# Kernel tuning notes

Hardware: AMD Instinct MI355X
Metric: run time of the kernel (lower is better)

The kernel has to match this reference:

```python
import jax, jax.numpy as jnp
import numpy as np

DT = 0.1
EPS = 0.01


def _trans_layer(x, W, b):
    # x: [B, 2U]; W: [U, U]; b: [U]
    U = b.shape[0]
    t = DT / EPS
    u_in, v_in = x[:, :U], x[:, U:]
    act = jnp.tanh(u_in)
    v_star = (v_in + t * act) / (1.0 + t)
    # Block matrix A = [[I, dt*W], [-dt*W^T, I]] -- identical for all samples,
    # so factor/solve ONCE with a multi-RHS solve instead of torch's per-sample batched LU.
    I = jnp.eye(U, dtype=x.dtype)
    A = jnp.block([[I, DT * W], [-DT * W.T, I]])  # [2U, 2U]
    rhs = jnp.concatenate([u_in + DT * b, v_star], axis=1)  # [B, 2U]
    y = jnp.linalg.solve(A, rhs.T).T  # [B, 2U]
    u, v = y[:, :U], y[:, U:]
    u_out = DT * (v @ W.T) - u_in - DT * b
    v_out = -DT * (u @ W) + t * v - v_in - t * act
    return jnp.concatenate([u_out, v_out], axis=1)


def setup_inputs() -> dict:
    key = jax.random.key(0)
    ks = jax.random.split(key, 14)
    B, D_IN, U, D_OUT = 32768, 256, 256, 10

    def lin_w(k, o, i):
        return (jax.random.uniform(k, (o, i), jnp.float32) * 2.0 - 1.0) / np.sqrt(i).astype(np.float32)

    def lin_b(k, o, fan_in):
        return (jax.random.uniform(k, (o,), jnp.float32) * 2.0 - 1.0) / np.sqrt(fan_in).astype(np.float32)

    return {
        'x': jax.random.normal(ks[0], (B, D_IN), jnp.float32),
        'Wi': lin_w(ks[1], U, D_IN), 'bi': lin_b(ks[2], U, D_IN),
        'W1': lin_w(ks[3], U, U), 'b1': lin_b(ks[4], U, U),
        'W2': lin_w(ks[5], U, U), 'b2': lin_b(ks[6], U, U),
        'W3': lin_w(ks[7], U, U), 'b3': lin_b(ks[8], U, U),
        'W4': lin_w(ks[9], U, U), 'b4': lin_b(ks[10], U, U),
        'Wo': lin_w(ks[11], D_OUT, U), 'bo': lin_b(ks[12], D_OUT, U),
    }


def reference(x, Wi, bi, W1, b1, W2, b2, W3, b3, W4, b4, Wo, bo):
    U = W1.shape[0]
    z = x @ Wi.T + bi                       # linearInput
    z = jnp.concatenate([z, jnp.tanh(z)], axis=1)  # [B, 2U]
    for W, b in ((W1, b1), (W2, b2), (W3, b3), (W4, b4)):
        z = _trans_layer(z, W, b)
    z = z[:, :U]
    logits = z @ Wo.T + bo                  # linearOutput
    return jax.nn.softmax(logits, axis=1)
```

## Files before the change

kernel.cpp:

```cpp
#include <hip/hip_runtime.h>
#include <math.h>

#define DTC 0.1f

typedef _Float16 half8 __attribute__((ext_vector_type(8)));
typedef _Float16 half4v __attribute__((ext_vector_type(4)));
typedef float f32x4 __attribute__((ext_vector_type(4)));
typedef float f32x2 __attribute__((ext_vector_type(2)));

__device__ __forceinline__ float fast_tanh(float x) {
  const float e = __expf(2.f * x);
  const float r = __builtin_amdgcn_rcpf(e + 1.f);
  return fmaf(-2.f, r, 1.f);
}


__global__ __launch_bounds__(256) void k_prep(
    const float* __restrict__ W0, const float* __restrict__ W1,
    const float* __restrict__ W2, const float* __restrict__ W3,
    const float* __restrict__ b2, const float* __restrict__ b3,
    const float* __restrict__ b4,
    _Float16* __restrict__ Wh, _Float16* __restrict__ Wt,
    float* __restrict__ crm) {
  const float* Ws[4] = {W0, W1, W2, W3};
  const int bid = blockIdx.x, tid = threadIdx.x;
  if (bid < 128) {
    const int t = bid * 256 + tid;
    const float* W = Ws[(t * 8) >> 16];
    const int off = (t * 8) & 65535;
    const float4 a = *(const float4*)&W[off];
    const float4 b = *(const float4*)&W[off + 4];
    half8 h;
    h[0] = (_Float16)a.x; h[1] = (_Float16)a.y; h[2] = (_Float16)a.z; h[3] = (_Float16)a.w;
    h[4] = (_Float16)b.x; h[5] = (_Float16)b.y; h[6] = (_Float16)b.z; h[7] = (_Float16)b.w;
    *(half8*)&Wh[t * 8] = h;
  } else if (bid < 384) {
    __shared__ float sh[32][33];
    const int b2i = bid - 128;
    const int l = b2i >> 6, t64 = b2i & 63;
    const int r0 = (t64 >> 3) * 32, c0 = (t64 & 7) * 32;
    const float* W = Ws[l];
    const int i = tid >> 5, j = tid & 31;
#pragma unroll
    for (int p = 0; p < 4; ++p)
      sh[p * 8 + i][j] = W[(r0 + p * 8 + i) * 256 + c0 + j];
    __syncthreads();
#pragma unroll
    for (int p = 0; p < 4; ++p)
      Wt[l * 65536 + (c0 + p * 8 + i) * 256 + r0 + j] = (_Float16)sh[j][p * 8 + i];
  } else {
    const int l = bid - 384;
    const float* W = Ws[l];
    const float* b = (l == 0) ? b2 : (l == 1) ? b3 : b4;
    float s = 0.f;
#pragma unroll 8
    for (int k = 0; k < 256; ++k) s = fmaf(b[k], W[k * 256 + tid], s);
    crm[l * 256 + tid] = -0.09f * s;
  }
}

__global__ __launch_bounds__(256) void k_smm3(const _Float16* __restrict__ A,
                                              const _Float16* __restrict__ B,
                                              const _Float16* __restrict__ Eadd,
                                              _Float16* __restrict__ C,
                                              float scale, int addI) {
  const int tid = threadIdx.x, wave = tid >> 6, lane = tid & 63;
  const int quad = lane >> 4, l16 = lane & 15;
  const int l = blockIdx.z;
  const _Float16* Al = A + (size_t)l * 65536;
  const _Float16* Bl = B + (size_t)l * 65536;
  _Float16* Cl = C + (size_t)l * 65536;
  const int m0 = blockIdx.y * 64 + wave * 16, n0 = blockIdx.x * 64;
  f32x4 acc[4] = {};
#pragma unroll
  for (int kt = 0; kt < 8; ++kt) {
    const half8 af = *(const half8*)&Al[(m0 + l16) * 256 + kt * 32 + quad * 8];
#pragma unroll
    for (int ni = 0; ni < 4; ++ni) {
      const half8 bf = *(const half8*)&Bl[(n0 + ni * 16 + l16) * 256 + kt * 32 + quad * 8];
      acc[ni] = __builtin_amdgcn_mfma_f32_16x16x32_f16(af, bf, acc[ni], 0, 0, 0);
    }
  }
#pragma unroll
  for (int ni = 0; ni < 4; ++ni)
#pragma unroll
    for (int r = 0; r < 4; ++r) {
      const int row = m0 + quad * 4 + r, col = n0 + ni * 16 + l16;
      float v = scale * acc[ni][r];
      if (addI) v += (row == col ? 1.f : 0.f) - (float)(Eadd + (size_t)l * 65536)[row * 256 + col];
      Cl[row * 256 + col] = (_Float16)v;
    }
}

__global__ __launch_bounds__(256) void k_pack(
    const _Float16* __restrict__ Ph, const _Float16* __restrict__ Qt,
    const _Float16* __restrict__ Wt, const float* __restrict__ Wi,
    const float* __restrict__ Wo,
    _Float16* __restrict__ PQP, _Float16* __restrict__ RmP,
    _Float16* __restrict__ WiP, _Float16* __restrict__ WoP) {
  const int t = blockIdx.x * 256 + threadIdx.x;
  if (t < 65536) {
    const int l = t >> 14, c = t & 16383;
    const int ntile = c >> 10, kt = (c >> 6) & 15, lb = c & 63;
    const int n = ntile * 16 + (lb & 15);
    const int kq = (lb >> 4) * 8;
    half8 h;
    if (kt < 8) {
      h = *(const half8*)&Ph[(size_t)l * 65536 + n * 256 + kt * 32 + kq];
#pragma unroll
      for (int j = 0; j < 8; ++j) h[j] = -h[j];
    } else {
      h = *(const half8*)&Qt[(size_t)l * 65536 + n * 256 + (kt - 8) * 32 + kq];
    }
    *(half8*)&PQP[(size_t)t * 8] = h;
  } else if (t < 90112) {
    const int tt = t - 65536;
    const int l = tt >> 13, c = tt & 8191;
    const int ntile = c >> 9, kt = (c >> 6) & 7, lb = c & 63;
    const int n = ntile * 16 + (lb & 15);
    const int k0 = kt * 32 + (lb >> 4) * 8;
    half8 h = *(const half8*)&Wt[(size_t)l * 65536 + n * 256 + k0];
#pragma unroll
    for (int j = 0; j < 8; ++j) h[j] = (_Float16)(-0.9f * (float)h[j]);
    *(half8*)&RmP[(size_t)tt * 8] = h;
  } else if (t < 98304) {
    const int c = t - 90112;
    const int ntile = c >> 9, kt = (c >> 6) & 7, lb = c & 63;
    const int n = ntile * 16 + (lb & 15);
    const int k0 = kt * 32 + (lb >> 4) * 8;
    const float4 a = *(const float4*)&Wi[n * 256 + k0];
    const float4 b = *(const float4*)&Wi[n * 256 + k0 + 4];
    half8 h;
    h[0] = (_Float16)a.x; h[1] = (_Float16)a.y; h[2] = (_Float16)a.z; h[3] = (_Float16)a.w;
    h[4] = (_Float16)b.x; h[5] = (_Float16)b.y; h[6] = (_Float16)b.z; h[7] = (_Float16)b.w;
    *(half8*)&WiP[(size_t)c * 8] = h;
  } else {
    const int c = t - 98304;
    const int kt = c >> 6, lb = c & 63;
    const int n = lb & 15;
    const int k0 = kt * 32 + (lb >> 4) * 8;
    half8 h;
#pragma unroll
    for (int j = 0; j < 8; ++j) h[j] = (_Float16)((n < 10) ? Wo[n * 256 + k0 + j] : 0.f);
    *(half8*)&WoP[(size_t)c * 8] = h;
  }
}


__device__ __forceinline__ int lds_off4(int row, int col0) {
  const int chunk = (col0 >> 3) ^ (row & 7);
  return row * 512 + (chunk << 4) + (col0 & 7) * 2;
}

template <int NKT, bool DUAL>
__device__ __forceinline__ void gemm_k(const _Float16* __restrict__ Bp,
                                       const _Float16* A1, const _Float16* A2,
                                       f32x4* acc, int wave, int lane, int quad, int l16) {
  half8 bf[4][2];
  auto loadB = [&](int kt, int s) {
#pragma unroll
    for (int ni = 0; ni < 2; ++ni)
      bf[s][ni] = *(const half8*)&Bp[(((wave * 2 + ni) * NKT + kt) * 64 + lane) * 8];
  };
  loadB(0, 0);
  loadB(1, 1);
  loadB(2, 2);
#pragma unroll
  for (int kt = 0; kt < NKT; ++kt) {
    const int s = kt & 3;
    if (kt + 3 < NKT) loadB(kt + 3, (kt + 3) & 3);
    const _Float16* Ab = (DUAL && kt >= NKT / 2) ? A2 : A1;
    const int akt = DUAL ? (kt & (NKT / 2 - 1)) : kt;
    half8 af[4];
#pragma unroll
    for (int mi = 0; mi < 4; ++mi) {
      const int row = mi * 16 + l16;
      const int chunk = (akt * 4 + quad) ^ (row & 7);
      af[mi] = *(const half8*)((const char*)Ab + row * 512 + (chunk << 4));
    }
    __builtin_amdgcn_s_setprio(1);
#pragma unroll
    for (int mi = 0; mi < 4; ++mi)
#pragma unroll
      for (int ni = 0; ni < 2; ++ni)
        acc[mi * 2 + ni] = __builtin_amdgcn_mfma_f32_16x16x32_f16(
            bf[s][ni], af[mi], acc[mi * 2 + ni], 0, 0, 0);
    __builtin_amdgcn_s_setprio(0);
  }
}

__global__ __launch_bounds__(512, 2) void k_fused(
    const float* __restrict__ x, const _Float16* __restrict__ WiP,
    const _Float16* __restrict__ PQP, const _Float16* __restrict__ RmP,
    const _Float16* __restrict__ WoP, const float* __restrict__ bi,
    const float* __restrict__ b1, const float* __restrict__ b2,
    const float* __restrict__ b3, const float* __restrict__ b4,
    const float* __restrict__ crm, const float* __restrict__ bo,
    float* __restrict__ out) {
  __shared__ __align__(16) _Float16 A1[64 * 256];
  __shared__ __align__(16) _Float16 A2[64 * 256];
  const int tid = threadIdx.x;
  const int wave = tid >> 6, lane = tid & 63;
  const int quad = lane >> 4, l16 = lane & 15;
  const int m0 = blockIdx.x * 64;

#pragma unroll
  for (int it = 0; it < 8; ++it) {
    const int idx = it * 512 + tid;
    const int row = idx >> 6, c4 = idx & 63;
    const float4 v = *(const float4*)&x[(size_t)(m0 + row) * 256 + c4 * 4];
    const int chunk = (c4 >> 1) ^ (row & 7), part = c4 & 1;
    _Float16* p = (_Float16*)((char*)A1 + row * 512 + (chunk << 4) + (part << 3));
    p[0] = (_Float16)v.x; p[1] = (_Float16)v.y; p[2] = (_Float16)v.z; p[3] = (_Float16)v.w;
  }
  __syncthreads();

  f32x4 acc[8];
  const f32x4 zero = {0.f, 0.f, 0.f, 0.f};
  half4v uph[8], r2p[8];

#pragma unroll
  for (int t = 0; t < 8; ++t) acc[t] = zero;
  gemm_k<8, false>(WiP, A1, A1, acc, wave, lane, quad, l16);
  __syncthreads();
#pragma unroll
  for (int ni = 0; ni < 2; ++ni) {
    const int col0 = wave * 32 + ni * 16 + quad * 4;
    const f32x4 bi4 = *(const f32x4*)&bi[col0];
    const f32x4 b14 = *(const f32x4*)&b1[col0];
#pragma unroll
    for (int mi = 0; mi < 4; ++mi) {
      const int row = mi * 16 + l16;
      const int off = lds_off4(row, col0);
      half4v h1, h2;
#pragma unroll
      for (int r = 0; r < 4; ++r) {
        const float z = acc[mi * 2 + ni][r] + bi4[r];
        h1[r] = (_Float16)(z + DTC * b14[r]);
        h2[r] = (_Float16)fast_tanh(z);
      }
      *(half4v*)((char*)A1 + off) = h1;
      *(half4v*)((char*)A2 + off) = h2;
      r2p[mi * 2 + ni] = h2;
    }
  }
  __syncthreads();

#pragma unroll 1
  for (int l = 0; l < 4; ++l) {
#pragma unroll
    for (int t = 0; t < 8; ++t) acc[t] = zero;
    gemm_k<16, true>(PQP + (size_t)l * 131072, A1, A2, acc, wave, lane, quad, l16);
    __syncthreads();
    const float* bn = (l == 0) ? b2 : (l == 1) ? b3 : b4;
#pragma unroll
    for (int ni = 0; ni < 2; ++ni) {
      const int col0 = wave * 32 + ni * 16 + quad * 4;
      f32x4 bn4 = zero;
      if (l < 3) bn4 = DTC * (*(const f32x4*)&bn[col0]);
#pragma unroll
      for (int mi = 0; mi < 4; ++mi) {
        const int row = mi * 16 + l16;
        const int off = lds_off4(row, col0);
        half4v hu, h1;
#pragma unroll
        for (int r = 0; r < 4; ++r) {
          const float u = acc[mi * 2 + ni][r];
          hu[r] = (_Float16)u;
          h1[r] = (_Float16)(u + bn4[r]);
        }
        uph[mi * 2 + ni] = hu;
        *(half4v*)((char*)A1 + off) = h1;
      }
    }
    __syncthreads();
    if (l < 3) {
#pragma unroll
      for (int t = 0; t < 8; ++t) acc[t] = zero;
      gemm_k<8, false>(RmP + (size_t)l * 65536, A1, A1, acc, wave, lane, quad, l16);
#pragma unroll
      for (int ni = 0; ni < 2; ++ni) {
        const int col0 = wave * 32 + ni * 16 + quad * 4;
        const f32x4 cc4 = *(const f32x4*)&crm[l * 256 + col0];
#pragma unroll
        for (int mi = 0; mi < 4; ++mi) {
          const int row = mi * 16 + l16;
          const int off = lds_off4(row, col0);
          half4v nr2;
#pragma unroll
          for (int r = 0; r < 4; ++r) {
            const float vp = acc[mi * 2 + ni][r] - cc4[r] - (float)r2p[mi * 2 + ni][r];
            nr2[r] = (_Float16)((vp + 10.f * fast_tanh((float)uph[mi * 2 + ni][r])) * (1.f / 11.f));
          }
          r2p[mi * 2 + ni] = nr2;
          *(half4v*)((char*)A2 + off) = nr2;
        }
      }
      __syncthreads();
    }
  }

  if (wave < 4) {
    f32x4 acch = zero;
#pragma unroll
    for (int kt = 0; kt < 8; ++kt) {
      const int row = wave * 16 + l16;
      const int chunk = (kt * 4 + quad) ^ (row & 7);
      const half8 af = *(const half8*)((const char*)A1 + row * 512 + (chunk << 4));
      const half8 bfr = *(const half8*)&WoP[(kt * 64 + lane) * 8];
      acch = __builtin_amdgcn_mfma_f32_16x16x32_f16(bfr, af, acch, 0, 0, 0);
    }
    float v4[4];
    float mx = -3.0e38f;
#pragma unroll
    for (int r = 0; r < 4; ++r) {
      const int cls = quad * 4 + r;
      const float v = acch[r] + ((cls < 10) ? bo[cls] : -3.0e38f);
      v4[r] = v;
      mx = fmaxf(mx, v);
    }
    mx = fmaxf(mx, __shfl_xor(mx, 16, 64));
    mx = fmaxf(mx, __shfl_xor(mx, 32, 64));
    float e4[4], s = 0.f;
#pragma unroll
    for (int r = 0; r < 4; ++r) {
      e4[r] = __expf(v4[r] - mx);
      s += e4[r];
    }
    s += __shfl_xor(s, 16, 64);
    s += __shfl_xor(s, 32, 64);
    const float rs = __builtin_amdgcn_rcpf(s);
    float* op = &out[(size_t)(m0 + wave * 16 + l16) * 10 + quad * 4];
    if (quad < 2) {
      f32x2 p0 = {e4[0] * rs, e4[1] * rs};
      f32x2 p1 = {e4[2] * rs, e4[3] * rs};
      *(f32x2*)op = p0;
      *(f32x2*)(op + 2) = p1;
    } else if (quad == 2) {
      f32x2 p0 = {e4[0] * rs, e4[1] * rs};
      *(f32x2*)op = p0;
    }
  }
}


extern "C" void kernel_launch(void* const* d_in, const int* in_sizes, int n_in,
                              void* d_out, int out_size, void* d_ws, size_t ws_size,
                              hipStream_t stream) {
  const float* x  = (const float*)d_in[0];
  const float* Wi = (const float*)d_in[1];
  const float* bi = (const float*)d_in[2];
  const float* W[4] = {(const float*)d_in[3], (const float*)d_in[5],
                       (const float*)d_in[7], (const float*)d_in[9]};
  const float* b[4] = {(const float*)d_in[4], (const float*)d_in[6],
                       (const float*)d_in[8], (const float*)d_in[10]};
  const float* Wo = (const float*)d_in[11];
  const float* bo = (const float*)d_in[12];
  float* out = (float*)d_out;

  const int Bsz = in_sizes[0] / 256;

  _Float16* hb = (_Float16*)d_ws;
  _Float16* WiP = hb;
  _Float16* WoP = hb + 65536;
  _Float16* PQP = hb + 69632;
  _Float16* RmP = hb + 593920;
  _Float16* Wh  = hb + 790528;
  _Float16* Wt  = hb + 1052672;
  _Float16* Eh  = hb + 1314816;
  _Float16* Ph  = hb + 1576960;
  _Float16* Qt  = hb + 1839104;
  float* crm = (float*)(hb + 2101248);

  const dim3 g64(4, 4, 4);
  k_prep<<<387, 256, 0, stream>>>(W[0], W[1], W[2], W[3], b[1], b[2], b[3],
                                  Wh, Wt, crm);
  k_smm3<<<g64, 256, 0, stream>>>(Wh, Wh, nullptr, Eh, 0.01f, 0);
  k_smm3<<<g64, 256, 0, stream>>>(Eh, Eh, Eh, Ph, 1.0f, 1);
  k_smm3<<<g64, 256, 0, stream>>>(Ph, Wt, nullptr, Qt, DTC, 0);
  k_pack<<<386, 256, 0, stream>>>(Ph, Qt, Wt, Wi, Wo, PQP, RmP, WiP, WoP);

  k_fused<<<Bsz / 64, 512, 0, stream>>>(x, WiP, PQP, RmP, WoP, bi,
                                        b[0], b[1], b[2], b[3], crm, bo, out);
}
```

Baseline: 184.6 us.

## Store LDS activations in MFMA fragment-native layout instead of swizzled row-major

Activation tiles in shared memory now sit in the exact per-lane order the MFMA A-fragment reads expect, so each fragment load is a contiguous lane*16 access with no XOR swizzle arithmetic. The x staging and epilogue writes are rewritten to scatter directly into this layout, each thread computing fixed base pointers once. This cuts address computation and should keep LDS reads conflict-free, but the half4 epilogue writes now use a different stride pattern that could introduce bank conflicts on the store side.

After: 186.4 us. No clear change (+1.0%).

```diff
diff --git a/kernel.cpp b/kernel.cpp
--- a/kernel.cpp
+++ b/kernel.cpp
@@ -147,10 +147,6 @@
 }
 
 
-__device__ __forceinline__ int lds_off4(int row, int col0) {
-  const int chunk = (col0 >> 3) ^ (row & 7);
-  return row * 512 + (chunk << 4) + (col0 & 7) * 2;
-}
 
 template <int NKT, bool DUAL>
 __device__ __forceinline__ void gemm_k(const _Float16* __restrict__ Bp,
@@ -165,19 +161,18 @@
   loadB(0, 0);
   loadB(1, 1);
   loadB(2, 2);
+  const char* a1b = (const char*)A1 + lane * 16;
+  const char* a2b = (const char*)A2 + lane * 16;
 #pragma unroll
   for (int kt = 0; kt < NKT; ++kt) {
     const int s = kt & 3;
     if (kt + 3 < NKT) loadB(kt + 3, (kt + 3) & 3);
-    const _Float16* Ab = (DUAL && kt >= NKT / 2) ? A2 : A1;
+    const char* Ab = (DUAL && kt >= NKT / 2) ? a2b : a1b;
     const int akt = DUAL ? (kt & (NKT / 2 - 1)) : kt;
     half8 af[4];
 #pragma unroll
-    for (int mi = 0; mi < 4; ++mi) {
-      const int row = mi * 16 + l16;
-      const int chunk = (akt * 4 + quad) ^ (row & 7);
-      af[mi] = *(const half8*)((const char*)Ab + row * 512 + (chunk << 4));
-    }
+    for (int mi = 0; mi < 4; ++mi)
+      af[mi] = *(const half8*)(Ab + (akt * 4 + mi) * 1024);
     __builtin_amdgcn_s_setprio(1);
 #pragma unroll
     for (int mi = 0; mi < 4; ++mi)
@@ -205,19 +200,23 @@
   const int m0 = blockIdx.x * 64;
 
 #pragma unroll
-  for (int it = 0; it < 8; ++it) {
-    const int idx = it * 512 + tid;
-    const int row = idx >> 6, c4 = idx & 63;
-    const float4 v = *(const float4*)&x[(size_t)(m0 + row) * 256 + c4 * 4];
-    const int chunk = (c4 >> 1) ^ (row & 7), part = c4 & 1;
-    _Float16* p = (_Float16*)((char*)A1 + row * 512 + (chunk << 4) + (part << 3));
-    p[0] = (_Float16)v.x; p[1] = (_Float16)v.y; p[2] = (_Float16)v.z; p[3] = (_Float16)v.w;
+  for (int mi = 0; mi < 4; ++mi) {
+    const size_t gb = (size_t)(m0 + mi * 16 + l16) * 256 + wave * 32 + quad * 8;
+    const float4 a = *(const float4*)&x[gb];
+    const float4 b = *(const float4*)&x[gb + 4];
+    half8 h;
+    h[0] = (_Float16)a.x; h[1] = (_Float16)a.y; h[2] = (_Float16)a.z; h[3] = (_Float16)a.w;
+    h[4] = (_Float16)b.x; h[5] = (_Float16)b.y; h[6] = (_Float16)b.z; h[7] = (_Float16)b.w;
+    *(half8*)((char*)A1 + ((wave * 4 + mi) * 64 + lane) * 16) = h;
   }
   __syncthreads();
 
   f32x4 acc[8];
   const f32x4 zero = {0.f, 0.f, 0.f, 0.f};
   half4v uph[8], r2p[8];
+
+  char* e1 = (char*)A1 + wave * 4096 + ((quad >> 1) * 16 + l16) * 16 + (quad & 1) * 8;
+  char* e2 = (char*)A2 + wave * 4096 + ((quad >> 1) * 16 + l16) * 16 + (quad & 1) * 8;
 
 #pragma unroll
   for (int t = 0; t < 8; ++t) acc[t] = zero;
@@ -230,8 +229,7 @@
     const f32x4 b14 = *(const f32x4*)&b1[col0];
 #pragma unroll
     for (int mi = 0; mi < 4; ++mi) {
-      const int row = mi * 16 + l16;
-      const int off = lds_off4(row, col0);
+      const int off = mi * 1024 + ni * 512;
       half4v h1, h2;
 #pragma unroll
       for (int r = 0; r < 4; ++r) {
@@ -239,8 +237,8 @@
         h1[r] = (_Float16)(z + DTC * b14[r]);
         h2[r] = (_Float16)fast_tanh(z);
       }
-      *(half4v*)((char*)A1 + off) = h1;
-      *(half4v*)((char*)A2 + off) = h2;
+      *(half4v*)(e1 + off) = h1;
+      *(half4v*)(e2 + off) = h2;
       r2p[mi * 2 + ni] = h2;
     }
   }
@@ -260,8 +258,7 @@
       if (l < 3) bn4 = DTC * (*(const f32x4*)&bn[col0]);
 #pragma unroll
       for (int mi = 0; mi < 4; ++mi) {
-        const int row = mi * 16 + l16;
-        const int off = lds_off4(row, col0);
+        const int off = mi * 1024 + ni * 512;
         half4v hu, h1;
 #pragma unroll
         for (int r = 0; r < 4; ++r) {
@@ -270,7 +267,7 @@
           h1[r] = (_Float16)(u + bn4[r]);
         }
         uph[mi * 2 + ni] = hu;
-        *(half4v*)((char*)A1 + off) = h1;
+        *(half4v*)(e1 + off) = h1;
       }
     }
     __syncthreads();
@@ -284,8 +281,7 @@
         const f32x4 cc4 = *(const f32x4*)&crm[l * 256 + col0];
 #pragma unroll
         for (int mi = 0; mi < 4; ++mi) {
-          const int row = mi * 16 + l16;
-          const int off = lds_off4(row, col0);
+          const int off = mi * 1024 + ni * 512;
           half4v nr2;
 #pragma unroll
           for (int r = 0; r < 4; ++r) {
@@ -293,7 +289,7 @@
             nr2[r] = (_Float16)((vp + 10.f * fast_tanh((float)uph[mi * 2 + ni][r])) * (1.f / 11.f));
           }
           r2p[mi * 2 + ni] = nr2;
-          *(half4v*)((char*)A2 + off) = nr2;
+          *(half4v*)(e2 + off) = nr2;
         }
       }
       __syncthreads();
@@ -304,9 +300,8 @@
     f32x4 acch = zero;
 #pragma unroll
     for (int kt = 0; kt < 8; ++kt) {
-      const int row = wave * 16 + l16;
-      const int chunk = (kt * 4 + quad) ^ (row & 7);
-      const half8 af = *(const half8*)((const char*)A1 + row * 512 + (chunk << 4));
+      const half8 af = *(const half8*)((const char*)A1 +
+                                       ((kt * 4 + wave) * 64 + lane) * 16);
       const half8 bfr = *(const half8*)&WoP[(kt * 64 + lane) * 8];
       acch = __builtin_amdgcn_mfma_f32_16x16x32_f16(bfr, af, acch, 0, 0, 0);
     }
```
